# Optimization experiments

Hardware: AMD Instinct MI355X
Metric: run time of the kernel (lower is better)

## Reference

```python
import jax, jax.numpy as jnp
import numpy as np

B, L, D = 4, 4096, 1024
H = 4
DK = D // H          # head key dim = 256
DV = D // H          # head value dim = 256
CHUNK = 32
CONV_K = 4
FIR_S, FIR_L = 5, 63
N_PATHS = 4
TAU_MIN = 0.25
HARD_FLOOR = 0.005
LEARN_FLOOR_MAX = 0.07
EPS = 1e-5


def _silu(x):
    return x * jax.nn.sigmoid(x)


def _l2norm(x):
    return x * jax.lax.rsqrt(jnp.sum(x * x, -1, keepdims=True) + 1e-6)


def _causal_dw_conv(x, filt):
    # x: (B, L, C); filt: (C, K). Depthwise causal conv1d.
    C, K = filt.shape
    xp = jnp.pad(x, ((0, 0), (K - 1, 0), (0, 0)))
    w = filt.T[:, None, :]  # (K, 1, C)
    return jax.lax.conv_general_dilated(xp, w, (1,), 'VALID',
                                        dimension_numbers=('NWC', 'WIO', 'NWC'),
                                        feature_group_count=C)


def _fir(x, filt):
    # x: (B, L, H, Dv); filt: (H, Dv, K)
    b, l, h, d = x.shape
    y = _causal_dw_conv(x.reshape(b, l, h * d), filt.reshape(h * d, filt.shape[-1]))
    return y.reshape(b, l, h, d)


def _delta_rule_chunkwise(q, k, v, beta):
    # q,k: (B,H,L,dk); v: (B,H,L,dv); beta: (B,H,L). L must be a multiple of CHUNK.
    b, h, Lq, dk = q.shape
    dv = v.shape[-1]
    q = _l2norm(q)
    k = _l2norm(k)
    v = v * beta[..., None]
    kb = k * beta[..., None]
    n = Lq // CHUNK
    r = lambda t: t.reshape(b, h, n, CHUNK, t.shape[-1])
    q, k, v, kb = r(q), r(k), r(v), r(kb)
    # A = strictly-lower part of -(k_beta @ k^T); the torch row loop computes
    # (I - A)^{-1} - I via forward substitution, then adds I back.
    A = -jnp.einsum('bhnid,bhnjd->bhnij', kb, k)
    A = jnp.tril(A, -1)
    eye = jnp.eye(CHUNK, dtype=q.dtype)
    Tinv = jax.scipy.linalg.solve_triangular(eye - A, jnp.broadcast_to(eye, A.shape),
                                             lower=True, unit_diagonal=True)
    u = Tinv @ v   # (b,h,n,c,dv)
    w = Tinv @ kb  # (b,h,n,c,dk)

    def step(S, inp):
        q_i, k_i, u_i, w_i = inp  # (b,h,c,d)
        attn = jnp.tril(jnp.einsum('bhid,bhjd->bhij', q_i, k_i))  # incl. diagonal
        u_adj = u_i - w_i @ S
        o_i = q_i @ S + attn @ u_adj
        S_new = S + jnp.einsum('bhcd,bhce->bhde', k_i, u_adj)
        return S_new, o_i

    S0 = jnp.zeros((b, h, dk, dv), dtype=q.dtype)
    xs = tuple(jnp.moveaxis(t, 2, 0) for t in (q, k, u, w))
    S, o = jax.lax.scan(step, S0, xs)
    o = jnp.moveaxis(o, 0, 2).reshape(b, h, Lq, dv)
    return o, S


def _stats(p):
    # p: (B,L,H,D) -> (B,L,H*4): mean, var (biased), mean|.|, l2 norm
    mean = p.mean(-1)
    var = p.var(-1)
    absm = jnp.abs(p).mean(-1)
    l2 = jnp.sqrt(jnp.sum(p * p, -1))
    s = jnp.stack([mean, var, absm, l2], -1)
    return s.reshape(p.shape[0], p.shape[1], -1)


def setup_inputs() -> dict:
    key = jax.random.key(0)
    ks = jax.random.split(key, 16)
    rn = lambda i, shape, s=0.02: jax.random.normal(ks[i], shape, jnp.float32) * s
    GATE_IN = D + 16 * H
    GATE_H = D * 2 // 2
    return {
        'hidden_states': jax.random.normal(ks[0], (B, L, D), jnp.float32),
        'Wq': rn(1, (D, D)), 'Wk': rn(2, (D, D)), 'Wv': rn(3, (D, D)),
        'Wb': rn(4, (H, D)),
        'conv_q_w': rn(5, (D, CONV_K), 0.2),
        'conv_k_w': rn(6, (D, CONV_K), 0.2),
        'conv_v_w': rn(7, (D, CONV_K), 0.2),
        'fir_short_w': rn(8, (H, DV, FIR_S)).at[..., -1].add(1.0),
        'fir_long_w': rn(9, (H, DV, FIR_L)).at[..., -1].add(1.0),
        'log_temp': jnp.zeros((H, N_PATHS), jnp.float32),
        'floor_param': jnp.full((H, N_PATHS), -2.0, jnp.float32),
        'gate_W1': rn(10, (GATE_H, GATE_IN)),
        'gate_b1': jnp.zeros((GATE_H,), jnp.float32),
        'gate_W2': rn(11, (H * N_PATHS, GATE_H)),
        'gate_b2': jnp.zeros((H * N_PATHS,), jnp.float32).at[N_PATHS - 1::N_PATHS].set(2.0),
        'o_norm_w': jnp.ones((DV,), jnp.float32),
        'Wo': rn(12, (D, D)),
    }


def reference(hidden_states, Wq, Wk, Wv, Wb, conv_q_w, conv_k_w, conv_v_w,
              fir_short_w, fir_long_w, log_temp, floor_param,
              gate_W1, gate_b1, gate_W2, gate_b2, o_norm_w, Wo):
    b, l, _ = hidden_states.shape
    # projections + short depthwise causal conv with silu activation
    q = _silu(_causal_dw_conv(hidden_states @ Wq.T, conv_q_w))
    k = _silu(_causal_dw_conv(hidden_states @ Wk.T, conv_k_w))
    v = _silu(_causal_dw_conv(hidden_states @ Wv.T, conv_v_w))
    beta = jax.nn.sigmoid(hidden_states @ Wb.T)  # (b,l,H)

    q_h = q.reshape(b, l, H, DK).transpose(0, 2, 1, 3)
    k_h = k.reshape(b, l, H, DK).transpose(0, 2, 1, 3)
    v_h = v.reshape(b, l, H, DV).transpose(0, 2, 1, 3)
    o_d, _S = _delta_rule_chunkwise(q_h, k_h, v_h, beta.transpose(0, 2, 1))
    path_delta = o_d.transpose(0, 2, 1, 3)  # (b,l,H,DV)

    v_direct = v.reshape(b, l, H, DV)
    path_short = _fir(v_direct, fir_short_w)
    path_long = _fir(v_direct, fir_long_w)

    gate_in = jnp.concatenate([hidden_states, _stats(path_short), _stats(path_long),
                               _stats(path_delta), _stats(v_direct)], -1)
    h1 = jax.nn.gelu(gate_in @ gate_W1.T + gate_b1, approximate=False)
    logits = (h1 @ gate_W2.T + gate_b2).reshape(b, l, H, N_PATHS)
    tau = jax.nn.softplus(log_temp) + TAU_MIN  # (H,4)
    probs = jax.nn.softmax(logits / tau, axis=-1)
    floor = jnp.minimum(HARD_FLOOR + jax.nn.sigmoid(floor_param) * LEARN_FLOOR_MAX, 0.25)
    sum_floor = jnp.minimum(jnp.sum(floor, -1, keepdims=True), 0.99)
    norm_floor = floor / sum_floor * 0.99
    clipped = jnp.maximum(probs, norm_floor + 1e-9)
    weights = clipped / (jnp.sum(clipped, -1, keepdims=True) + 1e-8)  # (b,l,H,4)

    paths = jnp.stack([path_short, path_long, path_delta, v_direct], axis=3)  # (b,l,H,4,DV)
    o = jnp.einsum('blhp,blhpd->blhd', weights, paths)
    o = o * jax.lax.rsqrt(jnp.mean(o * o, -1, keepdims=True) + EPS) * o_norm_w  # per-head RMSNorm
    return o.reshape(b, l, H * DV) @ Wo.T
```

## Files before the change

kernel.cpp:

```cpp
#include <hip/hip_runtime.h>
#include <hip/hip_bf16.h>
#include <cstddef>

#define NB 4
#define NL 4096
#define ND 1024
#define NH 4
#define NDK 256
#define NCH 128

typedef __hip_bfloat16 bf16;
typedef __attribute__((ext_vector_type(8))) short bf16x8;
typedef __attribute__((ext_vector_type(4))) float f32x4;

__device__ __forceinline__ float sigf(float x){ return 1.0f/(1.0f + expf(-x)); }
__device__ __forceinline__ float geluf(float x){ return 0.5f*x*(1.0f+erff(x*0.70710678118654752f)); }
__device__ __forceinline__ float us2f(unsigned short s){ return __uint_as_float(((unsigned int)s)<<16); }
__device__ __forceinline__ float b2f(bf16 x){ return __bfloat162float(x); }
__device__ __forceinline__ bf16  f2b(float x){ return __float2bfloat16(x); }
__device__ __forceinline__ unsigned short f2bu(float x){ bf16 h = f2b(x); return *(unsigned short*)&h; }

__device__ __forceinline__ float4 ld4f(const float* p){ return *(const float4*)p; }
__device__ __forceinline__ float4 ld4f(const bf16* p){
    ushort4 u = *(const ushort4*)p;
    return make_float4(us2f(u.x), us2f(u.y), us2f(u.z), us2f(u.w));
}
__device__ __forceinline__ void st4(float* p, float4 v){ *(float4*)p = v; }
__device__ __forceinline__ void st4(bf16* p, float4 v){
    bf16 a=f2b(v.x), b=f2b(v.y), c=f2b(v.z), d=f2b(v.w);
    ushort4 u;
    u.x=*(unsigned short*)&a; u.y=*(unsigned short*)&b;
    u.z=*(unsigned short*)&c; u.w=*(unsigned short*)&d;
    *(ushort4*)p = u;
}

#define DOT4(v, s) ((v).x*(s).x + (v).y*(s).y + (v).z*(s).z + (v).w*(s).w)

template<typename XT, int ACT, typename CT>
__global__ __launch_bounds__(256) void gemm_mfma(const XT* __restrict__ X,
    const float* __restrict__ W, const float* __restrict__ bias,
    CT* __restrict__ C, int M, int N, int K)
{
    constexpr int SX = (sizeof(XT)==4) ? 1 : 0;
    __shared__ unsigned short Ah[128*40];
    __shared__ unsigned short Al[SX ? 128*40 : 8];
    __shared__ unsigned short Bh[128*40];
    __shared__ unsigned short Bl[128*40];
    const int t = threadIdx.x;
    const int wid = t >> 6, l = t & 63;
    const int wr = wid >> 1, wc = wid & 1;
    const int bm = blockIdx.y*128, bn = blockIdx.x*128;
    const int sr = t >> 1, sk = (t & 1)*16;
    const XT* Xb = X + (size_t)(bm+sr)*K + sk;
    const float* Wb = W + (size_t)(bn+sr)*K + sk;
    const int lr = l & 15, lk = (l >> 4)*8;
    f32x4 acc[4][4];
    #pragma unroll
    for (int i=0;i<4;i++)
        #pragma unroll
        for (int j=0;j<4;j++) acc[i][j] = (f32x4){0.f,0.f,0.f,0.f};

    for (int kt = 0; kt < K; kt += 32) {
        unsigned short hx[16], lx[16], hw[16], lw[16];
        {
            float wf[16];
            *(float4*)&wf[0]  = ld4f(Wb + kt);
            *(float4*)&wf[4]  = ld4f(Wb + kt + 4);
            *(float4*)&wf[8]  = ld4f(Wb + kt + 8);
            *(float4*)&wf[12] = ld4f(Wb + kt + 12);
            #pragma unroll
            for (int j=0;j<16;j++){
                bf16 h = f2b(wf[j]);
                hw[j] = *(unsigned short*)&h;
                lw[j] = f2bu(wf[j] - b2f(h));
            }
        }
        if constexpr (SX){
            float xf[16];
            *(float4*)&xf[0]  = ld4f(Xb + kt);
            *(float4*)&xf[4]  = ld4f(Xb + kt + 4);
            *(float4*)&xf[8]  = ld4f(Xb + kt + 8);
            *(float4*)&xf[12] = ld4f(Xb + kt + 12);
            #pragma unroll
            for (int j=0;j<16;j++){
                bf16 h = f2b(xf[j]);
                hx[j] = *(unsigned short*)&h;
                lx[j] = f2bu(xf[j] - b2f(h));
            }
        } else {
            *(uint4*)&hx[0] = *(const uint4*)(Xb + kt);
            *(uint4*)&hx[8] = *(const uint4*)(Xb + kt + 8);
        }
        __syncthreads();
        *(uint4*)&Ah[sr*40 + sk]     = *(uint4*)&hx[0];
        *(uint4*)&Ah[sr*40 + sk + 8] = *(uint4*)&hx[8];
        if constexpr (SX){
            *(uint4*)&Al[sr*40 + sk]     = *(uint4*)&lx[0];
            *(uint4*)&Al[sr*40 + sk + 8] = *(uint4*)&lx[8];
        }
        *(uint4*)&Bh[sr*40 + sk]     = *(uint4*)&hw[0];
        *(uint4*)&Bh[sr*40 + sk + 8] = *(uint4*)&hw[8];
        *(uint4*)&Bl[sr*40 + sk]     = *(uint4*)&lw[0];
        *(uint4*)&Bl[sr*40 + sk + 8] = *(uint4*)&lw[8];
        __syncthreads();
        bf16x8 ah[4], al[4];
        #pragma unroll
        for (int mi=0;mi<4;mi++){
            ah[mi] = *(const bf16x8*)&Ah[(wr*64 + mi*16 + lr)*40 + lk];
            if constexpr (SX) al[mi] = *(const bf16x8*)&Al[(wr*64 + mi*16 + lr)*40 + lk];
        }
        #pragma unroll
        for (int nj=0;nj<4;nj++){
            bf16x8 bh = *(const bf16x8*)&Bh[(wc*64 + nj*16 + lr)*40 + lk];
            bf16x8 bl = *(const bf16x8*)&Bl[(wc*64 + nj*16 + lr)*40 + lk];
            #pragma unroll
            for (int mi=0;mi<4;mi++){
                acc[mi][nj] = __builtin_amdgcn_mfma_f32_16x16x32_bf16(ah[mi], bh, acc[mi][nj], 0,0,0);
                acc[mi][nj] = __builtin_amdgcn_mfma_f32_16x16x32_bf16(ah[mi], bl, acc[mi][nj], 0,0,0);
                if constexpr (SX)
                    acc[mi][nj] = __builtin_amdgcn_mfma_f32_16x16x32_bf16(al[mi], bh, acc[mi][nj], 0,0,0);
            }
        }
    }
    const int cr0 = (l >> 4) * 4;
    #pragma unroll
    for (int nj=0;nj<4;nj++){
        const int col = bn + wc*64 + nj*16 + lr;
        const float bv = bias ? bias[col] : 0.f;
        #pragma unroll
        for (int mi=0;mi<4;mi++){
            const int m0 = bm + wr*64 + mi*16 + cr0;
            #pragma unroll
            for (int r=0;r<4;r++){
                float v = acc[mi][nj][r] + bv;
                if (ACT==1) v = geluf(v);
                if constexpr (sizeof(CT)==2) C[(size_t)(m0+r)*N + col] = f2b(v);
                else                         C[(size_t)(m0+r)*N + col] = v;
            }
        }
    }
}

__global__ __launch_bounds__(256) void ftrans_kernel(const float* __restrict__ f,
    float* __restrict__ ft, int K)
{
    int idx = blockIdx.x*256 + threadIdx.x;
    if (idx < ND*K){
        int c = idx / K, k = idx - c*K;
        ft[k*ND + c] = f[idx];
    }
}

template<int K, int ACT>
__global__ __launch_bounds__(256) void dwconv3_kernel(const bf16* __restrict__ x,
    const float* __restrict__ ft, bf16* __restrict__ y)
{
    const int tr = threadIdx.x >> 7;
    const int c8 = (threadIdx.x & 127) * 8;
    const long row0 = (long)blockIdx.x * 16 + tr * 8;
    const int l0 = (int)(row0 & (NL - 1));
    const long bbase = row0 - l0;
    float xw[8][8];
    float acc[8][8];
    #pragma unroll
    for (int r=0;r<8;r++)
        #pragma unroll
        for (int j=0;j<8;j++) acc[r][j] = 0.f;
    #pragma unroll
    for (int w2=0;w2<8;w2++){
        int ls = l0 - (K-1) + w2;
        if (ls >= 0){
            const bf16* p = x + (bbase + ls)*ND + c8;
            ushort4 lo = *(const ushort4*)p;
            ushort4 hi = *(const ushort4*)(p + 4);
            xw[w2][0]=us2f(lo.x); xw[w2][1]=us2f(lo.y); xw[w2][2]=us2f(lo.z); xw[w2][3]=us2f(lo.w);
            xw[w2][4]=us2f(hi.x); xw[w2][5]=us2f(hi.y); xw[w2][6]=us2f(hi.z); xw[w2][7]=us2f(hi.w);
        } else {
            #pragma unroll
            for (int j=0;j<8;j++) xw[w2][j]=0.f;
        }
    }
    #pragma unroll
    for (int tt=0;tt<K;tt++){
        float4 f0 = *(const float4*)(ft + (size_t)tt*ND + c8);
        float4 f1 = *(const float4*)(ft + (size_t)tt*ND + c8 + 4);
        float fv[8] = {f0.x,f0.y,f0.z,f0.w,f1.x,f1.y,f1.z,f1.w};
        #pragma unroll
        for (int r=0;r<8;r++){
            const int sl = (tt + r) & 7;
            #pragma unroll
            for (int j=0;j<8;j++) acc[r][j] += xw[sl][j]*fv[j];
        }
        if (tt < K-1){
            const int sl = tt & 7;
            int ls = l0 - (K-1) + tt + 8;
            if (ls >= 0){
                const bf16* p = x + (bbase + ls)*ND + c8;
                ushort4 lo = *(const ushort4*)p;
                ushort4 hi = *(const ushort4*)(p + 4);
                xw[sl][0]=us2f(lo.x); xw[sl][1]=us2f(lo.y); xw[sl][2]=us2f(lo.z); xw[sl][3]=us2f(lo.w);
                xw[sl][4]=us2f(hi.x); xw[sl][5]=us2f(hi.y); xw[sl][6]=us2f(hi.z); xw[sl][7]=us2f(hi.w);
            } else {
                #pragma unroll
                for (int j=0;j<8;j++) xw[sl][j]=0.f;
            }
        }
    }
    #pragma unroll
    for (int r=0;r<8;r++){
        bf16* yp = y + (bbase + l0 + r)*ND + c8;
        float o[8];
        #pragma unroll
        for (int j=0;j<8;j++){
            float v = acc[r][j];
            if (ACT) v = v * sigf(v);
            o[j] = v;
        }
        st4(yp,   make_float4(o[0],o[1],o[2],o[3]));
        st4(yp+4, make_float4(o[4],o[5],o[6],o[7]));
    }
}

__global__ __launch_bounds__(256) void beta_kernel(const float* __restrict__ hs,
    const float* __restrict__ Wb, float* __restrict__ beta)
{
    const int wid = (int)((blockIdx.x*256 + threadIdx.x) >> 6);
    const int lane = threadIdx.x & 63;
    const int h = wid & 3, row = wid >> 2;
    const float* x = hs + (size_t)row*ND;
    const float* w = Wb + (size_t)h*ND;
    float s = 0.f;
    for (int i = lane; i < ND; i += 64) s += x[i]*w[i];
    #pragma unroll
    for (int o=32;o>0;o>>=1) s += __shfl_xor(s,o);
    if (lane == 0) beta[(size_t)row*NH + h] = sigf(s);
}

__global__ __launch_bounds__(256) void prep_kernel(bf16* __restrict__ q, bf16* __restrict__ k)
{
    const int row = blockIdx.x;
    const int h = threadIdx.x >> 6, lane = threadIdx.x & 63;
    const size_t off = (size_t)row*ND + h*NDK + lane*4;
    float4 q4 = ld4f(q + off);
    float4 k4 = ld4f(k + off);
    float sq = q4.x*q4.x+q4.y*q4.y+q4.z*q4.z+q4.w*q4.w;
    float sk = k4.x*k4.x+k4.y*k4.y+k4.z*k4.z+k4.w*k4.w;
    #pragma unroll
    for (int o=32;o>0;o>>=1){ sq += __shfl_xor(sq,o); sk += __shfl_xor(sk,o); }
    float rq = rsqrtf(sq + 1e-6f), rk = rsqrtf(sk + 1e-6f);
    q4.x*=rq; q4.y*=rq; q4.z*=rq; q4.w*=rq;
    k4.x*=rk; k4.y*=rk; k4.z*=rk; k4.w*=rk;
    st4(q + off, q4);
    st4(k + off, k4);
}

__global__ __launch_bounds__(256) void ut_kernel(const bf16* __restrict__ qn,
    const bf16* __restrict__ kn, const bf16* __restrict__ vv,
    const float* __restrict__ beta, bf16* __restrict__ u_,
    bf16* __restrict__ w_, bf16* __restrict__ attn)
{
    __shared__ float ks[32][257];
    __shared__ float qs[32][257];
    __shared__ float dkk[32][33];
    __shared__ float Ti[32][33];
    __shared__ float bs[32];
    const int blk = blockIdx.x;
    const int n = blk & (NCH-1), bh = blk >> 7;
    const int b = bh >> 2, h = bh & 3;
    const int t = threadIdx.x;
    const size_t base = ((size_t)b*NL + n*32)*ND + h*NDK;
    #pragma unroll
    for (int r=0;r<8;r++){
        int idx = t + (r<<8);
        int i = idx >> 6, dp = (idx & 63) << 2;
        float4 kv = ld4f(kn + base + (size_t)i*ND + dp);
        ks[i][dp]=kv.x; ks[i][dp+1]=kv.y; ks[i][dp+2]=kv.z; ks[i][dp+3]=kv.w;
        float4 qv = ld4f(qn + base + (size_t)i*ND + dp);
        qs[i][dp]=qv.x; qs[i][dp+1]=qv.y; qs[i][dp+2]=qv.z; qs[i][dp+3]=qv.w;
    }
    if (t < 32) bs[t] = beta[((size_t)b*NL + n*32 + t)*NH + h];
    __syncthreads();
    #pragma unroll
    for (int p=0;p<4;p++){
        const int i = (t>>5) + (p<<3), j = t & 31;
        float aK=0.f, aA=0.f;
        for (int d2=0; d2<256; d2++){
            float kj = ks[j][d2];
            aK += ks[i][d2]*kj;
            aA += qs[i][d2]*kj;
        }
        dkk[i][j] = aK;
        attn[((size_t)bh*NCH + n)*1024 + i*32 + j] = f2b((j<=i)? aA : 0.f);
    }
    __syncthreads();
    if (t < 32) Ti[0][t] = (t==0)?1.f:0.f;
    __syncthreads();
    for (int i=1;i<32;i++){
        if (t < 32){
            const int j = t;
            float v;
            if (j > i) v = 0.f;
            else if (j == i) v = 1.f;
            else {
                float acc = 0.f;
                for (int p2=j;p2<i;p2++) acc += dkk[i][p2]*Ti[p2][j];
                v = -bs[i]*acc;
            }
            Ti[i][j] = v;
        }
        __syncthreads();
    }
    {
        float ua[32];
        #pragma unroll
        for (int i=0;i<32;i++) ua[i]=0.f;
        for (int j=0;j<32;j++){
            float vj = b2f(vv[base + (size_t)j*ND + t]) * bs[j];
            #pragma unroll
            for (int i=0;i<32;i++) ua[i] += Ti[i][j]*vj;
        }
        #pragma unroll
        for (int i=0;i<32;i++) u_[base + (size_t)i*ND + t] = f2b(ua[i]);
        #pragma unroll
        for (int i=0;i<32;i++) ua[i]=0.f;
        for (int j=0;j<32;j++){
            float kjv = ks[j][t]*bs[j];
            #pragma unroll
            for (int i=0;i<32;i++) ua[i] += Ti[i][j]*kjv;
        }
        #pragma unroll
        for (int i=0;i<32;i++) w_[base + (size_t)i*ND + t] = f2b(ua[i]);
    }
}

__global__ __launch_bounds__(256) void scan16_kernel(const bf16* __restrict__ qn,
    const bf16* __restrict__ kn, const bf16* __restrict__ u_,
    const bf16* __restrict__ w_, const bf16* __restrict__ attn,
    bf16* __restrict__ pd)
{
    __shared__ float St[16][260];
    __shared__ unsigned short bw[32][268];
    __shared__ unsigned short bq[32][268];
    __shared__ unsigned short bk[32][268];
    __shared__ float ual[32][20];
    __shared__ float atl[32][33];
    const int blk = blockIdx.x;
    const int sl = blk & 15;
    const int bh = blk >> 4;
    const int b = bh >> 2, h = bh & 3;
    const int d0 = sl * 16;
    const int t = threadIdx.x;
    const int li = t & 31, dg = t >> 5;
    const int cg = t & 63, dh = t >> 6;
    for (int i = t; i < 16*260; i += 256) ((float*)St)[i] = 0.f;
    const bf16* qb = qn + (size_t)b*NL*ND + h*NDK;
    const bf16* kb = kn + (size_t)b*NL*ND + h*NDK;
    const bf16* ub = u_ + (size_t)b*NL*ND + h*NDK;
    const bf16* wb = w_ + (size_t)b*NL*ND + h*NDK;
    const bf16* ab = attn + (size_t)bh*NCH*1024;
    bf16* pdb = pd + (size_t)b*NL*ND + h*NDK + d0;
    for (int n=0;n<NCH;n++){
        const size_t cb = (size_t)n*32*ND;
        __syncthreads();
        #pragma unroll
        for (int j=0;j<32;j++) bw[j][t] = *(const unsigned short*)&wb[cb + (size_t)j*ND + t];
        #pragma unroll
        for (int j=0;j<32;j++) bq[j][t] = *(const unsigned short*)&qb[cb + (size_t)j*ND + t];
        #pragma unroll
        for (int j=0;j<32;j++) bk[j][t] = *(const unsigned short*)&kb[cb + (size_t)j*ND + t];
        #pragma unroll
        for (int r=0;r<4;r++){ int idx = t + (r<<8); atl[idx>>5][idx&31] = b2f(ab[(size_t)n*1024 + idx]); }
        __syncthreads();
        float ua0 = b2f(ub[cb + (size_t)li*ND + d0 + dg*2]);
        float ua1 = b2f(ub[cb + (size_t)li*ND + d0 + dg*2 + 1]);
        float o0 = 0.f, o1 = 0.f;
        for (int cgi=0; cgi<64; cgi++){
            ushort4 wv4 = *(const ushort4*)&bw[li][cgi*4];
            ushort4 qv4 = *(const ushort4*)&bq[li][cgi*4];
            float4 wv = make_float4(us2f(wv4.x),us2f(wv4.y),us2f(wv4.z),us2f(wv4.w));
            float4 qv = make_float4(us2f(qv4.x),us2f(qv4.y),us2f(qv4.z),us2f(qv4.w));
            float4 s0 = *(const float4*)&St[dg*2+0][cgi*4];
            float4 s1 = *(const float4*)&St[dg*2+1][cgi*4];
            ua0 -= DOT4(wv, s0);  ua1 -= DOT4(wv, s1);
            o0  += DOT4(qv, s0);  o1  += DOT4(qv, s1);
        }
        ual[li][dg*2]   = ua0;
        ual[li][dg*2+1] = ua1;
        __syncthreads();
        for (int j=0;j<32;j++){
            float av = atl[li][j];
            o0 += av*ual[j][dg*2];
            o1 += av*ual[j][dg*2+1];
        }
        {
            bf16 e0 = f2b(o0), e1 = f2b(o1);
            ushort2 st2;
            st2.x = *(unsigned short*)&e0; st2.y = *(unsigned short*)&e1;
            *(ushort2*)(pdb + (size_t)(n*32 + li)*ND + dg*2) = st2;
        }
        float4 sac[4];
        #pragma unroll
        for (int r=0;r<4;r++) sac[r] = make_float4(0.f,0.f,0.f,0.f);
        for (int j=0;j<32;j++){
            ushort4 kv4 = *(const ushort4*)&bk[j][cg*4];
            float4 kv = make_float4(us2f(kv4.x),us2f(kv4.y),us2f(kv4.z),us2f(kv4.w));
            float4 u4 = *(const float4*)&ual[j][dh*4];
            sac[0].x += kv.x*u4.x; sac[0].y += kv.y*u4.x; sac[0].z += kv.z*u4.x; sac[0].w += kv.w*u4.x;
            sac[1].x += kv.x*u4.y; sac[1].y += kv.y*u4.y; sac[1].z += kv.z*u4.y; sac[1].w += kv.w*u4.y;
            sac[2].x += kv.x*u4.z; sac[2].y += kv.y*u4.z; sac[2].z += kv.z*u4.z; sac[2].w += kv.w*u4.z;
            sac[3].x += kv.x*u4.w; sac[3].y += kv.y*u4.w; sac[3].z += kv.z*u4.w; sac[3].w += kv.w*u4.w;
        }
        #pragma unroll
        for (int r=0;r<4;r++){
            float4* sp = (float4*)&St[dh*4+r][cg*4];
            float4 cur = *sp;
            cur.x += sac[r].x; cur.y += sac[r].y; cur.z += sac[r].z; cur.w += sac[r].w;
            *sp = cur;
        }
    }
}

__global__ __launch_bounds__(256) void gate_in_kernel(const float* __restrict__ hs,
    const bf16* __restrict__ ps, const bf16* __restrict__ pl,
    const bf16* __restrict__ pdl, const bf16* __restrict__ vc,
    bf16* __restrict__ gin)
{
    const int row = blockIdx.x;
    const int t = threadIdx.x;
    const int h = t >> 6, lane = t & 63;
    float4 hv = ld4f(hs + (size_t)row*ND + t*4);
    st4(gin + (size_t)row*1088 + t*4, hv);
    const size_t off = (size_t)row*ND + h*NDK + lane*4;
    const bf16* srcs[4] = {ps, pl, pdl, vc};
    #pragma unroll
    for (int p=0;p<4;p++){
        float4 v = ld4f(srcs[p] + off);
        float sx = v.x+v.y+v.z+v.w;
        float sq = v.x*v.x+v.y*v.y+v.z*v.z+v.w*v.w;
        float sa = fabsf(v.x)+fabsf(v.y)+fabsf(v.z)+fabsf(v.w);
        #pragma unroll
        for (int o=32;o>0;o>>=1){ sx+=__shfl_xor(sx,o); sq+=__shfl_xor(sq,o); sa+=__shfl_xor(sa,o); }
        if (lane==0){
            float mean = sx*(1.f/256.f);
            float var  = sq*(1.f/256.f) - mean*mean;
            bf16* o2 = gin + (size_t)row*1088 + 1024 + p*16 + h*4;
            o2[0]=f2b(mean); o2[1]=f2b(var); o2[2]=f2b(sa*(1.f/256.f)); o2[3]=f2b(sqrtf(sq));
        }
    }
}

__global__ __launch_bounds__(256) void gate_weights_kernel(const bf16* __restrict__ h1,
    const float* __restrict__ W2, const float* __restrict__ b2,
    const float* __restrict__ log_temp, const float* __restrict__ fp,
    float* __restrict__ wt)
{
    __shared__ float part[16][17];
    __shared__ float lg[16];
    const int row = blockIdx.x, t = threadIdx.x;
    const int o = t >> 4, g = t & 15;
    const bf16* hr = h1 + (size_t)row*1024;
    const float* wr = W2 + (size_t)o*1024;
    float s = 0.f;
    for (int i2=0;i2<64;i2++){ int k = g + (i2<<4); s += b2f(hr[k])*wr[k]; }
    part[o][g] = s;
    __syncthreads();
    if (t < 16){
        float acc = b2[t];
        #pragma unroll
        for (int g2=0;g2<16;g2++) acc += part[t][g2];
        lg[t] = acc;
    }
    __syncthreads();
    if (t < 4){
        const int h = t;
        float x[4], fl[4];
        float mx = -1e30f;
        #pragma unroll
        for (int p=0;p<4;p++){
            float lt = log_temp[h*4+p];
            float tau = (lt > 20.f ? lt : log1pf(expf(lt))) + 0.25f;
            x[p] = lg[h*4+p] / tau;
            mx = fmaxf(mx, x[p]);
        }
        float se = 0.f;
        #pragma unroll
        for (int p=0;p<4;p++){ x[p] = expf(x[p]-mx); se += x[p]; }
        float sfl = 0.f;
        #pragma unroll
        for (int p=0;p<4;p++){
            fl[p] = fminf(0.005f + sigf(fp[h*4+p])*0.07f, 0.25f);
            sfl += fl[p];
        }
        float sf = fminf(sfl, 0.99f);
        float cs = 0.f;
        float cl[4];
        #pragma unroll
        for (int p=0;p<4;p++){
            float prob = x[p]/se;
            float nf = fl[p]/sf*0.99f;
            cl[p] = fmaxf(prob, nf + 1e-9f);
            cs += cl[p];
        }
        float inv = 1.f/(cs + 1e-8f);
        #pragma unroll
        for (int p=0;p<4;p++) wt[(size_t)row*16 + h*4 + p] = cl[p]*inv;
    }
}

__global__ __launch_bounds__(256) void mix_kernel(const float* wt,
    const bf16* ps, const bf16* pl, const bf16* pdl, const bf16* vc,
    const float* onw, bf16* om)
{
    const int row = blockIdx.x, t = threadIdx.x;
    const int h = t >> 6, lane = t & 63;
    const size_t off = (size_t)row*ND + h*NDK + lane*4;
    const float w0 = wt[(size_t)row*16+h*4+0];
    const float w1 = wt[(size_t)row*16+h*4+1];
    const float w2 = wt[(size_t)row*16+h*4+2];
    const float w3 = wt[(size_t)row*16+h*4+3];
    float4 a = ld4f(ps+off);
    float4 b4 = ld4f(pl+off);
    float4 c = ld4f(pdl+off);
    float4 d = ld4f(vc+off);
    float4 o;
    o.x = w0*a.x + w1*b4.x + w2*c.x + w3*d.x;
    o.y = w0*a.y + w1*b4.y + w2*c.y + w3*d.y;
    o.z = w0*a.z + w1*b4.z + w2*c.z + w3*d.z;
    o.w = w0*a.w + w1*b4.w + w2*c.w + w3*d.w;
    float sq = o.x*o.x+o.y*o.y+o.z*o.z+o.w*o.w;
    #pragma unroll
    for (int oo=32;oo>0;oo>>=1) sq += __shfl_xor(sq,oo);
    float r = rsqrtf(sq*(1.f/256.f) + 1e-5f);
    float4 nw = *(const float4*)(onw + lane*4);
    o.x *= r*nw.x; o.y *= r*nw.y; o.z *= r*nw.z; o.w *= r*nw.w;
    st4(om+off, o);
}

extern "C" void kernel_launch(void* const* d_in, const int* in_sizes, int n_in,
                              void* d_out, int out_size, void* d_ws, size_t ws_size,
                              hipStream_t stream)
{
    const float* hs  = (const float*)d_in[0];
    const float* Wq  = (const float*)d_in[1];
    const float* Wk  = (const float*)d_in[2];
    const float* Wv  = (const float*)d_in[3];
    const float* Wbp = (const float*)d_in[4];
    const float* cq  = (const float*)d_in[5];
    const float* ck  = (const float*)d_in[6];
    const float* cv  = (const float*)d_in[7];
    const float* fsw = (const float*)d_in[8];
    const float* flw = (const float*)d_in[9];
    const float* log_temp = (const float*)d_in[10];
    const float* floor_p  = (const float*)d_in[11];
    const float* gW1 = (const float*)d_in[12];
    const float* gb1 = (const float*)d_in[13];
    const float* gW2 = (const float*)d_in[14];
    const float* gb2 = (const float*)d_in[15];
    const float* onw = (const float*)d_in[16];
    const float* Wo  = (const float*)d_in[17];

    const size_t NEEDED = 206831616ULL;
    if (ws_size < NEEDED) return;

    const size_t E = 16777216ULL;
    bf16* W = (bf16*)d_ws;
    bf16* B0 = W;
    bf16* B1 = W + E;
    bf16* B2 = W + 2*E;
    bf16* B3 = W + 3*E;
    bf16* B4 = W + 4*E;
    bf16* B5 = W + 5*E;
    bf16* attnb = W + 6*E;
    bf16* gin = B4;
    bf16* h1  = B4 + 17825792;
    float* beta = (float*)((char*)d_ws + 205520896);
    float* wt   = (float*)((char*)d_ws + 205783040);
    float* ftc = (float*)attnb;
    float* fts = (float*)attnb;
    float* ftl = (float*)attnb + 8192;

    dim3 gg(8, 128);
    gemm_mfma<float,0,bf16><<<gg,256,0,stream>>>(hs, Wq, nullptr, B0, 16384, 1024, 1024);
    ftrans_kernel<<<16,256,0,stream>>>(cq, ftc, 4);
    dwconv3_kernel<4,1><<<1024,256,0,stream>>>(B0, ftc, B1);
    gemm_mfma<float,0,bf16><<<gg,256,0,stream>>>(hs, Wk, nullptr, B0, 16384, 1024, 1024);
    ftrans_kernel<<<16,256,0,stream>>>(ck, ftc, 4);
    dwconv3_kernel<4,1><<<1024,256,0,stream>>>(B0, ftc, B2);
    gemm_mfma<float,0,bf16><<<gg,256,0,stream>>>(hs, Wv, nullptr, B0, 16384, 1024, 1024);
    ftrans_kernel<<<16,256,0,stream>>>(cv, ftc, 4);
    dwconv3_kernel<4,1><<<1024,256,0,stream>>>(B0, ftc, B3);
    beta_kernel<<<16384,256,0,stream>>>(hs, Wbp, beta);
    prep_kernel<<<16384,256,0,stream>>>(B1, B2);
    ut_kernel<<<2048,256,0,stream>>>(B1, B2, B3, beta, B4, B5, attnb);
    scan16_kernel<<<256,256,0,stream>>>(B1, B2, B4, B5, attnb, B0);
    ftrans_kernel<<<20,256,0,stream>>>(fsw, fts, 5);
    dwconv3_kernel<5,0><<<1024,256,0,stream>>>(B3, fts, B1);
    ftrans_kernel<<<252,256,0,stream>>>(flw, ftl, 63);
    dwconv3_kernel<63,0><<<1024,256,0,stream>>>(B3, ftl, B2);
    gate_in_kernel<<<16384,256,0,stream>>>(hs, B1, B2, B0, B3, gin);
    gemm_mfma<bf16,1,bf16><<<gg,256,0,stream>>>(gin, gW1, gb1, h1, 16384, 1024, 1088);
    gate_weights_kernel<<<16384,256,0,stream>>>(h1, gW2, gb2, log_temp, floor_p, wt);
    mix_kernel<<<16384,256,0,stream>>>(wt, B1, B2, B0, B3, onw, B3);
    gemm_mfma<bf16,0,float><<<gg,256,0,stream>>>(B3, Wo, nullptr, (float*)d_out, 16384, 1024, 1024);
}
```

Baseline: 2.822 ms.

## Rewrite chunkwise delta-rule scan with MFMA and split-bf16 state

Replaces the scalar-FMA recurrent scan with a 128-thread kernel that runs the w@S, q@S, attn@u and k^T@u products on bf16 MFMA instructions. The fp32 state is kept in registers and mirrored into shared memory as a hi/lo bf16 pair, so the MFMAs keep near-fp32 accuracy at the cost of doubling the MFMA count. The block index mapping also changes so that consecutive blocks cover different batch-head pairs rather than different slices of one head. The aim is to cut the serial per-chunk compute that dominates this low-occupancy kernel; the risks are the split-precision error and the extra barriers and shared-memory transposes.

```diff
diff --git a/kernel.cpp b/kernel.cpp
--- a/kernel.cpp
+++ b/kernel.cpp
@@ -333,90 +333,126 @@
     }
 }
 
-__global__ __launch_bounds__(256) void scan16_kernel(const bf16* __restrict__ qn,
+__global__ __launch_bounds__(128) void scan_mfma_kernel(const bf16* __restrict__ qn,
     const bf16* __restrict__ kn, const bf16* __restrict__ u_,
     const bf16* __restrict__ w_, const bf16* __restrict__ attn,
     bf16* __restrict__ pd)
 {
-    __shared__ float St[16][260];
-    __shared__ unsigned short bw[32][268];
-    __shared__ unsigned short bq[32][268];
-    __shared__ unsigned short bk[32][268];
-    __shared__ float ual[32][20];
-    __shared__ float atl[32][33];
-    const int blk = blockIdx.x;
-    const int sl = blk & 15;
-    const int bh = blk >> 4;
+    __shared__ unsigned short ws_[32][264];
+    __shared__ unsigned short qs_[32][264];
+    __shared__ unsigned short kT_[256][40];
+    __shared__ unsigned short at_[32][40];
+    __shared__ unsigned short Shi_[16][264];
+    __shared__ unsigned short Slo_[16][264];
+    __shared__ unsigned short uh_[16][40];
+    __shared__ unsigned short ul_[16][40];
+    const int t = threadIdx.x;
+    const int wv = t >> 6, l = t & 63;
+    const int lr = l & 15, lg = l >> 4;
+    const int bid = blockIdx.x;
+    const int slice = bid >> 4, bh = bid & 15;
     const int b = bh >> 2, h = bh & 3;
-    const int d0 = sl * 16;
-    const int t = threadIdx.x;
-    const int li = t & 31, dg = t >> 5;
-    const int cg = t & 63, dh = t >> 6;
-    for (int i = t; i < 16*260; i += 256) ((float*)St)[i] = 0.f;
+    const int d0 = slice * 16;
     const bf16* qb = qn + (size_t)b*NL*ND + h*NDK;
     const bf16* kb = kn + (size_t)b*NL*ND + h*NDK;
     const bf16* ub = u_ + (size_t)b*NL*ND + h*NDK;
     const bf16* wb = w_ + (size_t)b*NL*ND + h*NDK;
     const bf16* ab = attn + (size_t)bh*NCH*1024;
     bf16* pdb = pd + (size_t)b*NL*ND + h*NDK + d0;
+    f32x4 Sreg[8];
+    #pragma unroll
+    for (int m=0;m<8;m++) Sreg[m] = (f32x4){0.f,0.f,0.f,0.f};
+    for (int i=t;i<16*264;i+=128){ ((unsigned short*)Shi_)[i]=0; ((unsigned short*)Slo_)[i]=0; }
+    __syncthreads();
     for (int n=0;n<NCH;n++){
         const size_t cb = (size_t)n*32*ND;
+        #pragma unroll
+        for (int it=0;it<16;++it){
+            int idx = it*128 + t;
+            int row = idx >> 6, c4 = (idx & 63)*4;
+            *(ushort4*)&ws_[row][c4] = *(const ushort4*)&wb[cb + (size_t)row*ND + c4];
+            *(ushort4*)&qs_[row][c4] = *(const ushort4*)&qb[cb + (size_t)row*ND + c4];
+            ushort4 kv = *(const ushort4*)&kb[cb + (size_t)row*ND + c4];
+            kT_[c4+0][row]=kv.x; kT_[c4+1][row]=kv.y; kT_[c4+2][row]=kv.z; kT_[c4+3][row]=kv.w;
+        }
+        #pragma unroll
+        for (int it=0;it<8;++it){
+            int idx = it*128 + t;
+            at_[idx>>5][idx&31] = *(const unsigned short*)&ab[(size_t)n*1024 + idx];
+        }
         __syncthreads();
-        #pragma unroll
-        for (int j=0;j<32;j++) bw[j][t] = *(const unsigned short*)&wb[cb + (size_t)j*ND + t];
-        #pragma unroll
-        for (int j=0;j<32;j++) bq[j][t] = *(const unsigned short*)&qb[cb + (size_t)j*ND + t];
-        #pragma unroll
-        for (int j=0;j<32;j++) bk[j][t] = *(const unsigned short*)&kb[cb + (size_t)j*ND + t];
-        #pragma unroll
-        for (int r=0;r<4;r++){ int idx = t + (r<<8); atl[idx>>5][idx&31] = b2f(ab[(size_t)n*1024 + idx]); }
+        f32x4 a0 = (f32x4){0.f,0.f,0.f,0.f};
+        f32x4 a1 = (f32x4){0.f,0.f,0.f,0.f};
+        {
+            const unsigned short (*Xs)[264] = wv ? qs_ : ws_;
+            #pragma unroll
+            for (int ks2=0; ks2<8; ++ks2){
+                bf16x8 sh  = *(const bf16x8*)&Shi_[lr][ks2*32 + lg*8];
+                bf16x8 slv = *(const bf16x8*)&Slo_[lr][ks2*32 + lg*8];
+                bf16x8 x0  = *(const bf16x8*)&Xs[lr][ks2*32 + lg*8];
+                bf16x8 x1  = *(const bf16x8*)&Xs[16+lr][ks2*32 + lg*8];
+                a0 = __builtin_amdgcn_mfma_f32_16x16x32_bf16(x0, sh,  a0, 0,0,0);
+                a0 = __builtin_amdgcn_mfma_f32_16x16x32_bf16(x0, slv, a0, 0,0,0);
+                a1 = __builtin_amdgcn_mfma_f32_16x16x32_bf16(x1, sh,  a1, 0,0,0);
+                a1 = __builtin_amdgcn_mfma_f32_16x16x32_bf16(x1, slv, a1, 0,0,0);
+            }
+        }
+        if (wv == 0){
+            #pragma unroll
+            for (int tile=0;tile<2;tile++){
+                #pragma unroll
+                for (int r=0;r<4;r++){
+                    int c = tile*16 + lg*4 + r;
+                    float uv = b2f(ub[cb + (size_t)c*ND + d0 + lr]);
+                    float ua = uv - (tile ? a1[r] : a0[r]);
+                    bf16 hi = f2b(ua);
+                    float lo = ua - b2f(hi);
+                    bf16 lob = f2b(lo);
+                    uh_[lr][c] = *(unsigned short*)&hi;
+                    ul_[lr][c] = *(unsigned short*)&lob;
+                }
+            }
+        }
         __syncthreads();
-        float ua0 = b2f(ub[cb + (size_t)li*ND + d0 + dg*2]);
-        float ua1 = b2f(ub[cb + (size_t)li*ND + d0 + dg*2 + 1]);
-        float o0 = 0.f, o1 = 0.f;
-        for (int cgi=0; cgi<64; cgi++){
-            ushort4 wv4 = *(const ushort4*)&bw[li][cgi*4];
-            ushort4 qv4 = *(const ushort4*)&bq[li][cgi*4];
-            float4 wv = make_float4(us2f(wv4.x),us2f(wv4.y),us2f(wv4.z),us2f(wv4.w));
-            float4 qv = make_float4(us2f(qv4.x),us2f(qv4.y),us2f(qv4.z),us2f(qv4.w));
-            float4 s0 = *(const float4*)&St[dg*2+0][cgi*4];
-            float4 s1 = *(const float4*)&St[dg*2+1][cgi*4];
-            ua0 -= DOT4(wv, s0);  ua1 -= DOT4(wv, s1);
-            o0  += DOT4(qv, s0);  o1  += DOT4(qv, s1);
-        }
-        ual[li][dg*2]   = ua0;
-        ual[li][dg*2+1] = ua1;
+        bf16x8 uA_h = *(const bf16x8*)&uh_[lr][lg*8];
+        bf16x8 uA_l = *(const bf16x8*)&ul_[lr][lg*8];
+        if (wv == 1){
+            bf16x8 at0 = *(const bf16x8*)&at_[lr][lg*8];
+            bf16x8 at1 = *(const bf16x8*)&at_[16+lr][lg*8];
+            a0 = __builtin_amdgcn_mfma_f32_16x16x32_bf16(at0, uA_h, a0, 0,0,0);
+            a0 = __builtin_amdgcn_mfma_f32_16x16x32_bf16(at0, uA_l, a0, 0,0,0);
+            a1 = __builtin_amdgcn_mfma_f32_16x16x32_bf16(at1, uA_h, a1, 0,0,0);
+            a1 = __builtin_amdgcn_mfma_f32_16x16x32_bf16(at1, uA_l, a1, 0,0,0);
+            #pragma unroll
+            for (int tile=0;tile<2;tile++){
+                #pragma unroll
+                for (int r=0;r<4;r++){
+                    int c = tile*16 + lg*4 + r;
+                    pdb[(size_t)(n*32 + c)*ND + lr] = f2b(tile ? a1[r] : a0[r]);
+                }
+            }
+        }
+        #pragma unroll
+        for (int m=0;m<8;m++){
+            bf16x8 kf = *(const bf16x8*)&kT_[wv*128 + m*16 + lr][lg*8];
+            Sreg[m] = __builtin_amdgcn_mfma_f32_16x16x32_bf16(uA_h, kf, Sreg[m], 0,0,0);
+            Sreg[m] = __builtin_amdgcn_mfma_f32_16x16x32_bf16(uA_l, kf, Sreg[m], 0,0,0);
+        }
+        #pragma unroll
+        for (int m=0;m<8;m++){
+            #pragma unroll
+            for (int r=0;r<4;r++){
+                float s = Sreg[m][r];
+                bf16 hi = f2b(s);
+                float lo = s - b2f(hi);
+                bf16 lob = f2b(lo);
+                int dv = lg*4 + r;
+                int dk = wv*128 + m*16 + lr;
+                Shi_[dv][dk] = *(unsigned short*)&hi;
+                Slo_[dv][dk] = *(unsigned short*)&lob;
+            }
+        }
         __syncthreads();
-        for (int j=0;j<32;j++){
-            float av = atl[li][j];
-            o0 += av*ual[j][dg*2];
-            o1 += av*ual[j][dg*2+1];
-        }
-        {
-            bf16 e0 = f2b(o0), e1 = f2b(o1);
-            ushort2 st2;
-            st2.x = *(unsigned short*)&e0; st2.y = *(unsigned short*)&e1;
-            *(ushort2*)(pdb + (size_t)(n*32 + li)*ND + dg*2) = st2;
-        }
-        float4 sac[4];
-        #pragma unroll
-        for (int r=0;r<4;r++) sac[r] = make_float4(0.f,0.f,0.f,0.f);
-        for (int j=0;j<32;j++){
-            ushort4 kv4 = *(const ushort4*)&bk[j][cg*4];
-            float4 kv = make_float4(us2f(kv4.x),us2f(kv4.y),us2f(kv4.z),us2f(kv4.w));
-            float4 u4 = *(const float4*)&ual[j][dh*4];
-            sac[0].x += kv.x*u4.x; sac[0].y += kv.y*u4.x; sac[0].z += kv.z*u4.x; sac[0].w += kv.w*u4.x;
-            sac[1].x += kv.x*u4.y; sac[1].y += kv.y*u4.y; sac[1].z += kv.z*u4.y; sac[1].w += kv.w*u4.y;
-            sac[2].x += kv.x*u4.z; sac[2].y += kv.y*u4.z; sac[2].z += kv.z*u4.z; sac[2].w += kv.w*u4.z;
-            sac[3].x += kv.x*u4.w; sac[3].y += kv.y*u4.w; sac[3].z += kv.z*u4.w; sac[3].w += kv.w*u4.w;
-        }
-        #pragma unroll
-        for (int r=0;r<4;r++){
-            float4* sp = (float4*)&St[dh*4+r][cg*4];
-            float4 cur = *sp;
-            cur.x += sac[r].x; cur.y += sac[r].y; cur.z += sac[r].z; cur.w += sac[r].w;
-            *sp = cur;
-        }
     }
 }
 
@@ -592,7 +628,7 @@
     beta_kernel<<<16384,256,0,stream>>>(hs, Wbp, beta);
     prep_kernel<<<16384,256,0,stream>>>(B1, B2);
     ut_kernel<<<2048,256,0,stream>>>(B1, B2, B3, beta, B4, B5, attnb);
-    scan16_kernel<<<256,256,0,stream>>>(B1, B2, B4, B5, attnb, B0);
+    scan_mfma_kernel<<<256,128,0,stream>>>(B1, B2, B4, B5, attnb, B0);
     ftrans_kernel<<<20,256,0,stream>>>(fsw, fts, 5);
     dwconv3_kernel<5,0><<<1024,256,0,stream>>>(B3, fts, B1);
     ftrans_kernel<<<252,256,0,stream>>>(flw, ftl, 63);
```

Result: slower. 4.079 ms (+44.5%).

## Split delta-rule scan into 8-column slices and vectorize chunk loads

Applied to the files above, without the earlier changes.

The chunkwise delta-rule scan kernel now gives each block 8 value columns instead of 16, which doubles the grid from 256 to 512 blocks. The goal is more concurrent work per CU on a latency-bound sequential scan, and shorter per-chunk critical paths. The per-chunk shared-memory staging of w, q and k now uses ushort4 vector loads instead of scalar 16-bit loads. The cost is that every block re-reads the full q/k/w chunk tiles, so redundant global and shared-memory traffic doubles.

```diff
diff --git a/kernel.cpp b/kernel.cpp
--- a/kernel.cpp
+++ b/kernel.cpp
@@ -333,26 +333,26 @@
     }
 }
 
-__global__ __launch_bounds__(256) void scan16_kernel(const bf16* __restrict__ qn,
+__global__ __launch_bounds__(256) void scan8_kernel(const bf16* __restrict__ qn,
     const bf16* __restrict__ kn, const bf16* __restrict__ u_,
     const bf16* __restrict__ w_, const bf16* __restrict__ attn,
     bf16* __restrict__ pd)
 {
-    __shared__ float St[16][260];
     __shared__ unsigned short bw[32][268];
     __shared__ unsigned short bq[32][268];
     __shared__ unsigned short bk[32][268];
-    __shared__ float ual[32][20];
+    __shared__ float St[8][260];
+    __shared__ float ual[32][12];
     __shared__ float atl[32][33];
     const int blk = blockIdx.x;
-    const int sl = blk & 15;
-    const int bh = blk >> 4;
+    const int sl = blk >> 4;
+    const int bh = blk & 15;
     const int b = bh >> 2, h = bh & 3;
-    const int d0 = sl * 16;
+    const int d0 = sl * 8;
     const int t = threadIdx.x;
     const int li = t & 31, dg = t >> 5;
     const int cg = t & 63, dh = t >> 6;
-    for (int i = t; i < 16*260; i += 256) ((float*)St)[i] = 0.f;
+    for (int i = t; i < 8*260; i += 256) ((float*)St)[i] = 0.f;
     const bf16* qb = qn + (size_t)b*NL*ND + h*NDK;
     const bf16* kb = kn + (size_t)b*NL*ND + h*NDK;
     const bf16* ub = u_ + (size_t)b*NL*ND + h*NDK;
@@ -363,59 +363,50 @@
         const size_t cb = (size_t)n*32*ND;
         __syncthreads();
         #pragma unroll
-        for (int j=0;j<32;j++) bw[j][t] = *(const unsigned short*)&wb[cb + (size_t)j*ND + t];
-        #pragma unroll
-        for (int j=0;j<32;j++) bq[j][t] = *(const unsigned short*)&qb[cb + (size_t)j*ND + t];
-        #pragma unroll
-        for (int j=0;j<32;j++) bk[j][t] = *(const unsigned short*)&kb[cb + (size_t)j*ND + t];
+        for (int it=0;it<8;++it){
+            int idx = it*256 + t;
+            int row = idx >> 6, c4 = (idx & 63)*4;
+            *(ushort4*)&bw[row][c4] = *(const ushort4*)&wb[cb + (size_t)row*ND + c4];
+            *(ushort4*)&bq[row][c4] = *(const ushort4*)&qb[cb + (size_t)row*ND + c4];
+            *(ushort4*)&bk[row][c4] = *(const ushort4*)&kb[cb + (size_t)row*ND + c4];
+        }
         #pragma unroll
         for (int r=0;r<4;r++){ int idx = t + (r<<8); atl[idx>>5][idx&31] = b2f(ab[(size_t)n*1024 + idx]); }
         __syncthreads();
-        float ua0 = b2f(ub[cb + (size_t)li*ND + d0 + dg*2]);
-        float ua1 = b2f(ub[cb + (size_t)li*ND + d0 + dg*2 + 1]);
-        float o0 = 0.f, o1 = 0.f;
+        float uaAcc = b2f(ub[cb + (size_t)li*ND + d0 + dg]);
+        float oAcc = 0.f;
         for (int cgi=0; cgi<64; cgi++){
             ushort4 wv4 = *(const ushort4*)&bw[li][cgi*4];
             ushort4 qv4 = *(const ushort4*)&bq[li][cgi*4];
             float4 wv = make_float4(us2f(wv4.x),us2f(wv4.y),us2f(wv4.z),us2f(wv4.w));
             float4 qv = make_float4(us2f(qv4.x),us2f(qv4.y),us2f(qv4.z),us2f(qv4.w));
-            float4 s0 = *(const float4*)&St[dg*2+0][cgi*4];
-            float4 s1 = *(const float4*)&St[dg*2+1][cgi*4];
-            ua0 -= DOT4(wv, s0);  ua1 -= DOT4(wv, s1);
-            o0  += DOT4(qv, s0);  o1  += DOT4(qv, s1);
-        }
-        ual[li][dg*2]   = ua0;
-        ual[li][dg*2+1] = ua1;
+            float4 s = *(const float4*)&St[dg][cgi*4];
+            uaAcc -= DOT4(wv, s);
+            oAcc  += DOT4(qv, s);
+        }
+        ual[li][dg] = uaAcc;
         __syncthreads();
-        for (int j=0;j<32;j++){
-            float av = atl[li][j];
-            o0 += av*ual[j][dg*2];
-            o1 += av*ual[j][dg*2+1];
-        }
-        {
-            bf16 e0 = f2b(o0), e1 = f2b(o1);
-            ushort2 st2;
-            st2.x = *(unsigned short*)&e0; st2.y = *(unsigned short*)&e1;
-            *(ushort2*)(pdb + (size_t)(n*32 + li)*ND + dg*2) = st2;
-        }
-        float4 sac[4];
-        #pragma unroll
-        for (int r=0;r<4;r++) sac[r] = make_float4(0.f,0.f,0.f,0.f);
+        for (int j=0;j<32;j++) oAcc += atl[li][j]*ual[j][dg];
+        pdb[(size_t)(n*32 + li)*ND + dg] = f2b(oAcc);
+        float4 sac0 = make_float4(0.f,0.f,0.f,0.f);
+        float4 sac1 = make_float4(0.f,0.f,0.f,0.f);
         for (int j=0;j<32;j++){
             ushort4 kv4 = *(const ushort4*)&bk[j][cg*4];
             float4 kv = make_float4(us2f(kv4.x),us2f(kv4.y),us2f(kv4.z),us2f(kv4.w));
-            float4 u4 = *(const float4*)&ual[j][dh*4];
-            sac[0].x += kv.x*u4.x; sac[0].y += kv.y*u4.x; sac[0].z += kv.z*u4.x; sac[0].w += kv.w*u4.x;
-            sac[1].x += kv.x*u4.y; sac[1].y += kv.y*u4.y; sac[1].z += kv.z*u4.y; sac[1].w += kv.w*u4.y;
-            sac[2].x += kv.x*u4.z; sac[2].y += kv.y*u4.z; sac[2].z += kv.z*u4.z; sac[2].w += kv.w*u4.z;
-            sac[3].x += kv.x*u4.w; sac[3].y += kv.y*u4.w; sac[3].z += kv.z*u4.w; sac[3].w += kv.w*u4.w;
-        }
-        #pragma unroll
-        for (int r=0;r<4;r++){
-            float4* sp = (float4*)&St[dh*4+r][cg*4];
-            float4 cur = *sp;
-            cur.x += sac[r].x; cur.y += sac[r].y; cur.z += sac[r].z; cur.w += sac[r].w;
-            *sp = cur;
+            float u0 = ual[j][dh*2];
+            float u1 = ual[j][dh*2+1];
+            sac0.x += kv.x*u0; sac0.y += kv.y*u0; sac0.z += kv.z*u0; sac0.w += kv.w*u0;
+            sac1.x += kv.x*u1; sac1.y += kv.y*u1; sac1.z += kv.z*u1; sac1.w += kv.w*u1;
+        }
+        {
+            float4* sp0 = (float4*)&St[dh*2+0][cg*4];
+            float4 c0 = *sp0;
+            c0.x += sac0.x; c0.y += sac0.y; c0.z += sac0.z; c0.w += sac0.w;
+            *sp0 = c0;
+            float4* sp1 = (float4*)&St[dh*2+1][cg*4];
+            float4 c1 = *sp1;
+            c1.x += sac1.x; c1.y += sac1.y; c1.z += sac1.z; c1.w += sac1.w;
+            *sp1 = c1;
         }
     }
 }
@@ -592,7 +583,7 @@
     beta_kernel<<<16384,256,0,stream>>>(hs, Wbp, beta);
     prep_kernel<<<16384,256,0,stream>>>(B1, B2);
     ut_kernel<<<2048,256,0,stream>>>(B1, B2, B3, beta, B4, B5, attnb);
-    scan16_kernel<<<256,256,0,stream>>>(B1, B2, B4, B5, attnb, B0);
+    scan8_kernel<<<512,256,0,stream>>>(B1, B2, B4, B5, attnb, B0);
     ftrans_kernel<<<20,256,0,stream>>>(fsw, fts, 5);
     dwconv3_kernel<5,0><<<1024,256,0,stream>>>(B3, fts, B1);
     ftrans_kernel<<<252,256,0,stream>>>(flw, ftl, 63);
```

After: 2.783 ms. Within noise of the previous version (-1.4%).
